# Optimization experiments

Measured on AMD Instinct MI355X. Metric: run time of the kernel, lower is better.

Reference implementation:

```python
import jax, jax.numpy as jnp
import numpy as np

BLOCK = 32  # mxfp8 block size along K


def setup_inputs() -> dict:
    key = jax.random.key(0)
    ks = jax.random.split(key, 7)
    TOK, IN, OUT, RANK = 8192, 4096, 4096, 64
    return {
        "input": jax.random.normal(ks[0], (TOK, IN), dtype=jnp.float32),
        "weight_q": jax.random.normal(ks[1], (OUT, IN), dtype=jnp.float32),
        "block_scale": jax.random.uniform(ks[2], (OUT, IN // BLOCK), dtype=jnp.float32),
        "bias": jax.random.normal(ks[3], (OUT,), dtype=jnp.float32),
        "svd_u": jax.random.normal(ks[4], (OUT, RANK), dtype=jnp.float32),
        "svd_s": jax.random.uniform(ks[5], (RANK,), dtype=jnp.float32),
        "svd_v": jax.random.normal(ks[6], (IN, RANK), dtype=jnp.float32),
    }


def _dequant_mxfp8(weight_q, block_scale):
    # weight_q: [M, K], block_scale: [M, K//BLOCK] -> per-block scaled weight [M, K]
    M, K = weight_q.shape
    nb = K // BLOCK
    w = weight_q.reshape(M, nb, BLOCK) * block_scale.reshape(M, nb, 1)
    return w.reshape(M, K)


def reference(input, weight_q, block_scale, bias, svd_u, svd_s, svd_v):
    # SVD outlier branch: ((input @ V) * S) @ U^T
    outlier = ((input @ svd_v) * svd_s[None, :]) @ svd_u.T  # [TOK, OUT]
    # Dequantize mxfp8 weight then linear: input @ W^T + bias
    w = _dequant_mxfp8(weight_q, block_scale)
    residual = input @ w.T + bias[None, :]
    return outlier + residual
```

## Files before the change

### kernel.cpp

```cpp
#include <hip/hip_runtime.h>
#include <stdint.h>

typedef unsigned short ushort_t;
typedef __attribute__((ext_vector_type(8))) short short8;
typedef __attribute__((ext_vector_type(4))) unsigned short ushort4_t;
typedef __attribute__((ext_vector_type(8))) unsigned short ushort8;
typedef __attribute__((ext_vector_type(4))) float f32x4;

#define TOK 8192
#define DIM_IN 4096
#define DIM_OUT 4096
#define RANK 64
#define NT (DIM_IN / 64)

__device__ __forceinline__ ushort_t f2bf(float f) {
    unsigned u = __float_as_uint(f);
    unsigned r = (u + 0x7fffu + ((u >> 16) & 1u)) >> 16;
    return (ushort_t)r;
}
__device__ __forceinline__ float bf2f(ushort_t u) {
    return __uint_as_float(((unsigned)u) << 16);
}

__device__ __forceinline__ void gload16(const void* g, void* l) {
    __builtin_amdgcn_global_load_lds(
        (const __attribute__((address_space(1))) unsigned int*)g,
        (__attribute__((address_space(3))) unsigned int*)l,
        16, 0, 0);
}

__global__ __launch_bounds__(256) void prep_input_k(const float* __restrict__ in,
                                                    ushort_t* __restrict__ out) {
    size_t idx = (size_t)blockIdx.x * 256 + threadIdx.x;
    const float4* p = (const float4*)(in + idx * 8);
    float4 f0 = p[0], f1 = p[1];
    ushort8 o;
    o[0] = f2bf(f0.x); o[1] = f2bf(f0.y); o[2] = f2bf(f0.z); o[3] = f2bf(f0.w);
    o[4] = f2bf(f1.x); o[5] = f2bf(f1.y); o[6] = f2bf(f1.z); o[7] = f2bf(f1.w);
    *(ushort8*)(out + idx * 8) = o;
}

__global__ __launch_bounds__(256) void prep_weight_k(const float* __restrict__ wq,
                                                     const float* __restrict__ scale,
                                                     const float* __restrict__ U,
                                                     const float* __restrict__ s,
                                                     const float* __restrict__ V,
                                                     ushort_t* __restrict__ Wb) {
    __shared__ ushort_t sm[18432];
    const int tid = threadIdx.x;
    const int wv = tid >> 6;
    const int lane = tid & 63;
    const int ob = blockIdx.x >> 5;
    const int kb = blockIdx.x & 31;

    char* smb = (char*)sm;
#pragma unroll
    for (int j = 0; j < 8; ++j) {
        int idx = j * 256 + tid;
        int row = idx >> 4;
        int c4 = idx & 15;
        float4 sv = *(const float4*)&s[c4 * 4];
        float4 u = *(const float4*)&U[(size_t)(ob * 128 + row) * RANK + c4 * 4];
        ushort4_t up;
        up[0] = f2bf(u.x * sv.x); up[1] = f2bf(u.y * sv.y);
        up[2] = f2bf(u.z * sv.z); up[3] = f2bf(u.w * sv.w);
        int wbyte = row * 128 + ((c4 * 8) ^ ((row & 7) << 4));
        *(ushort4_t*)(smb + wbyte) = up;
        float4 v = *(const float4*)&V[(size_t)(kb * 128 + row) * RANK + c4 * 4];
        ushort4_t vp;
        vp[0] = f2bf(v.x); vp[1] = f2bf(v.y); vp[2] = f2bf(v.z); vp[3] = f2bf(v.w);
        *(ushort4_t*)(smb + 16384 + wbyte) = vp;
    }
    __syncthreads();

    const int wr = wv >> 1, wc = wv & 1;
    f32x4 acc[4][4] = {};
    {
        short8 a[4], b[4];
#pragma unroll
        for (int kk = 0; kk < 2; ++kk) {
#pragma unroll
            for (int f = 0; f < 4; ++f) {
                int r = wr * 64 + f * 16 + (lane & 15);
                int kbyte = ((lane >> 4) * 16 + kk * 64) ^ ((r & 7) << 4);
                a[f] = *(const short8*)(smb + r * 128 + kbyte);
                int r2 = wc * 64 + f * 16 + (lane & 15);
                int kbyte2 = ((lane >> 4) * 16 + kk * 64) ^ ((r2 & 7) << 4);
                b[f] = *(const short8*)(smb + 16384 + r2 * 128 + kbyte2);
            }
#pragma unroll
            for (int fm = 0; fm < 4; ++fm)
#pragma unroll
                for (int fn = 0; fn < 4; ++fn)
                    acc[fm][fn] = __builtin_amdgcn_mfma_f32_16x16x32_bf16(
                        a[fm], b[fn], acc[fm][fn], 0, 0, 0);
        }
    }
    __syncthreads();

#pragma unroll
    for (int fm = 0; fm < 4; ++fm)
#pragma unroll
        for (int fn = 0; fn < 4; ++fn) {
            int row0 = wr * 64 + fm * 16 + (lane >> 4) * 4;
            int col = wc * 64 + fn * 16 + (lane & 15);
#pragma unroll
            for (int r = 0; r < 4; ++r)
                sm[(row0 + r) * 136 + col] = f2bf(acc[fm][fn][r]);
        }
    __syncthreads();

    const int ty = tid >> 4, tx = tid & 15;
#pragma unroll
    for (int i = 0; i < 8; ++i) {
        int ol = ty * 8 + i;
        int o = ob * 128 + ol;
        int k0 = kb * 128 + tx * 8;
        float sc = scale[(size_t)o * (DIM_IN / 32) + (k0 >> 5)];
        float4 q0 = *(const float4*)&wq[(size_t)o * DIM_IN + k0];
        float4 q1 = *(const float4*)&wq[(size_t)o * DIM_IN + k0 + 4];
        ushort8 sv8 = *(const ushort8*)&sm[ol * 136 + tx * 8];
        ushort8 w;
        w[0] = f2bf(q0.x * sc + bf2f(sv8[0]));
        w[1] = f2bf(q0.y * sc + bf2f(sv8[1]));
        w[2] = f2bf(q0.z * sc + bf2f(sv8[2]));
        w[3] = f2bf(q0.w * sc + bf2f(sv8[3]));
        w[4] = f2bf(q1.x * sc + bf2f(sv8[4]));
        w[5] = f2bf(q1.y * sc + bf2f(sv8[5]));
        w[6] = f2bf(q1.z * sc + bf2f(sv8[6]));
        w[7] = f2bf(q1.w * sc + bf2f(sv8[7]));
        *(ushort8*)&Wb[(size_t)o * DIM_IN + k0] = w;
    }
}

__global__ __launch_bounds__(512, 2) void gemm_k(const ushort_t* __restrict__ A,
                                                 const ushort_t* __restrict__ B,
                                                 const float* __restrict__ bias,
                                                 float* __restrict__ C) {
    __shared__ ushort_t lds[2][2][2][8192];

    const int tid = threadIdx.x;
    const int wid = tid >> 6;
    const int lane = tid & 63;

    int bid = blockIdx.x;
    int swz = (bid & 7) * 64 + (bid >> 3);
    const int bm = swz >> 4;
    const int bn = swz & 15;

    const int wr = wid >> 2;
    const int wc = wid & 3;

    const int lane2 = lane ^ (((lane >> 5) & 1) << 1);
    const int srow = (wid >> 1) * 16 + (lane2 >> 2);
    const int scol = (wid & 1) * 32 + (lane2 & 3) * 8;
    const ushort_t* pa = A + (size_t)(bm * 256 + srow) * DIM_IN + scol;
    const ushort_t* pb = B + (size_t)(bn * 256 + srow) * DIM_IN + scol;

    const int loff = ((((lane & 15) * 64 + (lane >> 4) * 16) ^ (((lane >> 3) & 1) << 5)) >> 1);

    f32x4 acc[8][4] = {};

    auto stageA = [&](int buf, int half, int t) {
        const ushort_t* g = pa + (size_t)half * 128 * DIM_IN + t * 64;
        gload16(g, &lds[buf][0][half][wid * 512]);
        gload16(g + (size_t)64 * DIM_IN, &lds[buf][0][half][(wid + 8) * 512]);
    };
    auto stageB = [&](int buf, int half, int t) {
        const ushort_t* g = pb + (size_t)half * 128 * DIM_IN + t * 64;
        gload16(g, &lds[buf][1][half][wid * 512]);
        gload16(g + (size_t)64 * DIM_IN, &lds[buf][1][half][(wid + 8) * 512]);
    };

    auto tile_step = [&](int buf, int t, int mode) {
        const ushort_t* LA = &lds[buf][0][wr][0];
        const ushort_t* LB = &lds[buf][1][wc >> 1][0];
        const int bsub = (wc & 1) * 4;
        short8 aA[4], aB[4], bA[2][2], bB[2][2];

        auto rdA = [&](short8 (&dst)[4], int mhalf, int kk) {
#pragma unroll
            for (int m = 0; m < 4; ++m)
                dst[m] = *(const short8*)(LA + ((((mhalf * 4 + m) * 2) + kk) << 9) + loff);
        };
        auto rdB = [&](short8 (&dst)[2][2], int noff, int kk) {
#pragma unroll
            for (int n = 0; n < 2; ++n)
                dst[n][kk] = *(const short8*)(LB + ((((bsub + noff + n) * 2) + kk) << 9) + loff);
        };
        auto cluster = [&](short8 (&av)[4], short8 (&bv)[2][2], int kk, int mb, int nb) {
            __builtin_amdgcn_s_setprio(1);
#pragma unroll
            for (int m = 0; m < 4; ++m)
#pragma unroll
                for (int n = 0; n < 2; ++n)
                    acc[mb + m][nb + n] =
                        __builtin_amdgcn_mfma_f32_16x16x32_bf16(av[m], bv[n][kk], acc[mb + m][nb + n], 0, 0, 0);
            __builtin_amdgcn_s_setprio(0);
        };

        rdA(aA, 0, 0);
        rdB(bA, 0, 0);
        rdA(aB, 0, 1);
        rdB(bA, 0, 1);
        if (mode >= 1) stageA(buf ^ 1, 1, t + 1);
        cluster(aA, bA, 0, 0, 0);
        rdB(bB, 2, 0);
        cluster(aB, bA, 1, 0, 0);

        rdB(bB, 2, 1);
        cluster(aA, bB, 0, 0, 2);
        rdA(aA, 1, 0);
        cluster(aB, bB, 1, 0, 2);
        __builtin_amdgcn_s_barrier();

        rdA(aB, 1, 1);
        if (mode == 2) { stageB(buf, 0, t + 2); stageB(buf, 1, t + 2); }
        cluster(aA, bB, 0, 4, 2);
        cluster(aB, bB, 1, 4, 2);
        __builtin_amdgcn_s_barrier();

        if (mode == 2) stageA(buf, 0, t + 2);
        cluster(aA, bA, 0, 4, 0);
        cluster(aB, bA, 1, 4, 0);
        if (mode == 2)
            asm volatile("s_waitcnt vmcnt(6)" ::: "memory");
        else if (mode == 1)
            asm volatile("s_waitcnt vmcnt(0)" ::: "memory");
        if (mode >= 1) __builtin_amdgcn_s_barrier();
    };

    stageA(0, 0, 0); stageA(0, 1, 0); stageB(0, 0, 0); stageB(0, 1, 0);
    stageB(1, 0, 1); stageB(1, 1, 1); stageA(1, 0, 1);
    asm volatile("s_waitcnt vmcnt(6)" ::: "memory");
    __builtin_amdgcn_s_barrier();

    for (int t = 0; t < NT - 2; t += 2) {
        tile_step(0, t, 2);
        tile_step(1, t + 1, 2);
    }
    tile_step(0, NT - 2, 1);
    tile_step(1, NT - 1, 0);

    const int ccol = lane & 15;
    const int crow = (lane >> 4) * 4;
#pragma unroll
    for (int n = 0; n < 4; ++n) {
        int gcol = bn * 256 + wc * 64 + n * 16 + ccol;
        float bv = bias[gcol];
#pragma unroll
        for (int m = 0; m < 8; ++m) {
            size_t grow = (size_t)(bm * 256 + wr * 128 + m * 16 + crow);
#pragma unroll
            for (int r = 0; r < 4; ++r)
                C[(grow + r) * DIM_OUT + gcol] = acc[m][n][r] + bv;
        }
    }
}

extern "C" void kernel_launch(void* const* d_in, const int* in_sizes, int n_in,
                              void* d_out, int out_size, void* d_ws, size_t ws_size,
                              hipStream_t stream) {
    const float* input = (const float*)d_in[0];
    const float* wq    = (const float*)d_in[1];
    const float* scale = (const float*)d_in[2];
    const float* bias  = (const float*)d_in[3];
    const float* U     = (const float*)d_in[4];
    const float* s     = (const float*)d_in[5];
    const float* V     = (const float*)d_in[6];
    float* out = (float*)d_out;

    ushort_t* Abf = (ushort_t*)d_ws;
    ushort_t* Wbf = Abf + (size_t)TOK * DIM_IN;

    prep_input_k<<<(TOK * DIM_IN) / (256 * 8), 256, 0, stream>>>(input, Abf);
    prep_weight_k<<<(DIM_OUT / 128) * (DIM_IN / 128), 256, 0, stream>>>(wq, scale, U, s, V, Wbf);
    gemm_k<<<(TOK / 256) * (DIM_OUT / 256), 512, 0, stream>>>(Abf, Wbf, bias, out);
}
```

Baseline: 286.7 us.

## Simplify GEMM to 256x128 tiles with 4 waves and K=32 double buffering

Replaces the 256x256 block tile (8 waves, hand-interleaved MFMA clusters and staggered async loads over K=64 stages) with a 256x128 tile using 4 waves and a plain double-buffered loop over K=32 stages. Each iteration loads all A/B fragments then issues 32 MFMAs, waiting for all outstanding loads and barriering per stage. This reduces scheduling complexity and LDS use, but halves the B-tile reuse per block, doubles the number of k-steps and barriers, and loses the fine-grained overlap of loads with compute.

```diff
diff --git a/kernel.cpp b/kernel.cpp
--- a/kernel.cpp
+++ b/kernel.cpp
@@ -11,7 +11,7 @@
 #define DIM_IN 4096
 #define DIM_OUT 4096
 #define RANK 64
-#define NT (DIM_IN / 64)
+#define NT32 (DIM_IN / 32)
 
 __device__ __forceinline__ ushort_t f2bf(float f) {
     unsigned u = __float_as_uint(f);
@@ -133,120 +133,83 @@
     }
 }
 
-__global__ __launch_bounds__(512, 2) void gemm_k(const ushort_t* __restrict__ A,
+__global__ __launch_bounds__(256, 2) void gemm_k(const ushort_t* __restrict__ A,
                                                  const ushort_t* __restrict__ B,
                                                  const float* __restrict__ bias,
                                                  float* __restrict__ C) {
-    __shared__ ushort_t lds[2][2][2][8192];
+    __shared__ ushort_t lds[2][12288];
 
     const int tid = threadIdx.x;
     const int wid = tid >> 6;
     const int lane = tid & 63;
 
     int bid = blockIdx.x;
-    int swz = (bid & 7) * 64 + (bid >> 3);
-    const int bm = swz >> 4;
-    const int bn = swz & 15;
-
-    const int wr = wid >> 2;
-    const int wc = wid & 3;
+    int swz = (bid & 7) * 128 + (bid >> 3);
+    const int bm = swz >> 5;
+    const int bn = swz & 31;
+
+    const int wr = wid >> 1;
+    const int wc = wid & 1;
 
     const int lane2 = lane ^ (((lane >> 5) & 1) << 1);
-    const int srow = (wid >> 1) * 16 + (lane2 >> 2);
-    const int scol = (wid & 1) * 32 + (lane2 & 3) * 8;
-    const ushort_t* pa = A + (size_t)(bm * 256 + srow) * DIM_IN + scol;
-    const ushort_t* pb = B + (size_t)(bn * 256 + srow) * DIM_IN + scol;
+    const int sr = lane2 >> 2;
+    const int sc = (lane2 & 3) * 8;
+    const ushort_t* pa = A + (size_t)(bm * 256 + sr) * DIM_IN + sc;
+    const ushort_t* pb = B + (size_t)(bn * 128 + sr) * DIM_IN + sc;
 
     const int loff = ((((lane & 15) * 64 + (lane >> 4) * 16) ^ (((lane >> 3) & 1) << 5)) >> 1);
 
     f32x4 acc[8][4] = {};
 
-    auto stageA = [&](int buf, int half, int t) {
-        const ushort_t* g = pa + (size_t)half * 128 * DIM_IN + t * 64;
-        gload16(g, &lds[buf][0][half][wid * 512]);
-        gload16(g + (size_t)64 * DIM_IN, &lds[buf][0][half][(wid + 8) * 512]);
+    auto stage = [&](int buf, int t) {
+#pragma unroll
+        for (int j = 0; j < 4; ++j) {
+            int s = wid * 4 + j;
+            gload16(pa + (size_t)(s * 16) * DIM_IN + t * 32, &lds[buf][s * 512]);
+        }
+#pragma unroll
+        for (int j = 0; j < 2; ++j) {
+            int s = wid * 2 + j;
+            gload16(pb + (size_t)(s * 16) * DIM_IN + t * 32, &lds[buf][8192 + s * 512]);
+        }
     };
-    auto stageB = [&](int buf, int half, int t) {
-        const ushort_t* g = pb + (size_t)half * 128 * DIM_IN + t * 64;
-        gload16(g, &lds[buf][1][half][wid * 512]);
-        gload16(g + (size_t)64 * DIM_IN, &lds[buf][1][half][(wid + 8) * 512]);
-    };
-
-    auto tile_step = [&](int buf, int t, int mode) {
-        const ushort_t* LA = &lds[buf][0][wr][0];
-        const ushort_t* LB = &lds[buf][1][wc >> 1][0];
-        const int bsub = (wc & 1) * 4;
-        short8 aA[4], aB[4], bA[2][2], bB[2][2];
-
-        auto rdA = [&](short8 (&dst)[4], int mhalf, int kk) {
-#pragma unroll
-            for (int m = 0; m < 4; ++m)
-                dst[m] = *(const short8*)(LA + ((((mhalf * 4 + m) * 2) + kk) << 9) + loff);
-        };
-        auto rdB = [&](short8 (&dst)[2][2], int noff, int kk) {
-#pragma unroll
-            for (int n = 0; n < 2; ++n)
-                dst[n][kk] = *(const short8*)(LB + ((((bsub + noff + n) * 2) + kk) << 9) + loff);
-        };
-        auto cluster = [&](short8 (&av)[4], short8 (&bv)[2][2], int kk, int mb, int nb) {
-            __builtin_amdgcn_s_setprio(1);
-#pragma unroll
-            for (int m = 0; m < 4; ++m)
-#pragma unroll
-                for (int n = 0; n < 2; ++n)
-                    acc[mb + m][nb + n] =
-                        __builtin_amdgcn_mfma_f32_16x16x32_bf16(av[m], bv[n][kk], acc[mb + m][nb + n], 0, 0, 0);
-            __builtin_amdgcn_s_setprio(0);
-        };
-
-        rdA(aA, 0, 0);
-        rdB(bA, 0, 0);
-        rdA(aB, 0, 1);
-        rdB(bA, 0, 1);
-        if (mode >= 1) stageA(buf ^ 1, 1, t + 1);
-        cluster(aA, bA, 0, 0, 0);
-        rdB(bB, 2, 0);
-        cluster(aB, bA, 1, 0, 0);
-
-        rdB(bB, 2, 1);
-        cluster(aA, bB, 0, 0, 2);
-        rdA(aA, 1, 0);
-        cluster(aB, bB, 1, 0, 2);
-        __builtin_amdgcn_s_barrier();
-
-        rdA(aB, 1, 1);
-        if (mode == 2) { stageB(buf, 0, t + 2); stageB(buf, 1, t + 2); }
-        cluster(aA, bB, 0, 4, 2);
-        cluster(aB, bB, 1, 4, 2);
-        __builtin_amdgcn_s_barrier();
-
-        if (mode == 2) stageA(buf, 0, t + 2);
-        cluster(aA, bA, 0, 4, 0);
-        cluster(aB, bA, 1, 4, 0);
-        if (mode == 2)
-            asm volatile("s_waitcnt vmcnt(6)" ::: "memory");
-        else if (mode == 1)
+
+    stage(0, 0);
+    asm volatile("s_waitcnt vmcnt(0)" ::: "memory");
+    __builtin_amdgcn_s_barrier();
+
+    for (int t = 0; t < NT32; ++t) {
+        const int cur = t & 1;
+        if (t + 1 < NT32) stage(cur ^ 1, t + 1);
+
+        const ushort_t* L = &lds[cur][0];
+        short8 a[8], b[4];
+#pragma unroll
+        for (int m = 0; m < 8; ++m)
+            a[m] = *(const short8*)(L + (wr * 8 + m) * 512 + loff);
+#pragma unroll
+        for (int n = 0; n < 4; ++n)
+            b[n] = *(const short8*)(L + 8192 + (wc * 4 + n) * 512 + loff);
+
+        __builtin_amdgcn_s_setprio(1);
+#pragma unroll
+        for (int m = 0; m < 8; ++m)
+#pragma unroll
+            for (int n = 0; n < 4; ++n)
+                acc[m][n] = __builtin_amdgcn_mfma_f32_16x16x32_bf16(a[m], b[n], acc[m][n], 0, 0, 0);
+        __builtin_amdgcn_s_setprio(0);
+
+        if (t + 1 < NT32) {
             asm volatile("s_waitcnt vmcnt(0)" ::: "memory");
-        if (mode >= 1) __builtin_amdgcn_s_barrier();
-    };
-
-    stageA(0, 0, 0); stageA(0, 1, 0); stageB(0, 0, 0); stageB(0, 1, 0);
-    stageB(1, 0, 1); stageB(1, 1, 1); stageA(1, 0, 1);
-    asm volatile("s_waitcnt vmcnt(6)" ::: "memory");
-    __builtin_amdgcn_s_barrier();
-
-    for (int t = 0; t < NT - 2; t += 2) {
-        tile_step(0, t, 2);
-        tile_step(1, t + 1, 2);
-    }
-    tile_step(0, NT - 2, 1);
-    tile_step(1, NT - 1, 0);
+            __builtin_amdgcn_s_barrier();
+        }
+    }
 
     const int ccol = lane & 15;
     const int crow = (lane >> 4) * 4;
 #pragma unroll
     for (int n = 0; n < 4; ++n) {
-        int gcol = bn * 256 + wc * 64 + n * 16 + ccol;
+        int gcol = bn * 128 + wc * 64 + n * 16 + ccol;
         float bv = bias[gcol];
 #pragma unroll
         for (int m = 0; m < 8; ++m) {
@@ -275,5 +238,5 @@
 
     prep_input_k<<<(TOK * DIM_IN) / (256 * 8), 256, 0, stream>>>(input, Abf);
     prep_weight_k<<<(DIM_OUT / 128) * (DIM_IN / 128), 256, 0, stream>>>(wq, scale, U, s, V, Wbf);
-    gemm_k<<<(TOK / 256) * (DIM_OUT / 256), 512, 0, stream>>>(Abf, Wbf, bias, out);
-}
+    gemm_k<<<(TOK / 256) * (DIM_OUT / 128), 256, 0, stream>>>(Abf, Wbf, bias, out);
+}
```

Result: slower. 362.8 us (+26.5%).

## Replace interleaved staged prefetch with simple double-buffered stage/consume loop

Applied to the files above, without the earlier changes.

Replaces the finely interleaved schedule, where A and B tile loads for later K-steps were issued between MFMA clusters with mid-tile barriers, with a plain double-buffer loop. Each iteration now consumes the current buffer, hits a barrier, then issues all eight loads for tile t+2 into that buffer before waiting. This simplifies synchronisation and removes the intra-tile barriers. In exchange, global loads are no longer spread across the MFMA work and the wait comes right after issuing the loads, so latency hiding may be weaker.

```diff
diff --git a/kernel.cpp b/kernel.cpp
--- a/kernel.cpp
+++ b/kernel.cpp
@@ -161,18 +161,19 @@
 
     f32x4 acc[8][4] = {};
 
-    auto stageA = [&](int buf, int half, int t) {
-        const ushort_t* g = pa + (size_t)half * 128 * DIM_IN + t * 64;
-        gload16(g, &lds[buf][0][half][wid * 512]);
-        gload16(g + (size_t)64 * DIM_IN, &lds[buf][0][half][(wid + 8) * 512]);
+    auto stage = [&](int buf, int t) {
+#pragma unroll
+        for (int half = 0; half < 2; ++half) {
+            const ushort_t* ga = pa + (size_t)half * 128 * DIM_IN + t * 64;
+            gload16(ga, &lds[buf][0][half][wid * 512]);
+            gload16(ga + (size_t)64 * DIM_IN, &lds[buf][0][half][(wid + 8) * 512]);
+            const ushort_t* gb = pb + (size_t)half * 128 * DIM_IN + t * 64;
+            gload16(gb, &lds[buf][1][half][wid * 512]);
+            gload16(gb + (size_t)64 * DIM_IN, &lds[buf][1][half][(wid + 8) * 512]);
+        }
     };
-    auto stageB = [&](int buf, int half, int t) {
-        const ushort_t* g = pb + (size_t)half * 128 * DIM_IN + t * 64;
-        gload16(g, &lds[buf][1][half][wid * 512]);
-        gload16(g + (size_t)64 * DIM_IN, &lds[buf][1][half][(wid + 8) * 512]);
-    };
-
-    auto tile_step = [&](int buf, int t, int mode) {
+
+    auto consume = [&](int buf) {
         const ushort_t* LA = &lds[buf][0][wr][0];
         const ushort_t* LB = &lds[buf][1][wc >> 1][0];
         const int bsub = (wc & 1) * 4;
@@ -203,44 +204,38 @@
         rdB(bA, 0, 0);
         rdA(aB, 0, 1);
         rdB(bA, 0, 1);
-        if (mode >= 1) stageA(buf ^ 1, 1, t + 1);
         cluster(aA, bA, 0, 0, 0);
         rdB(bB, 2, 0);
         cluster(aB, bA, 1, 0, 0);
-
         rdB(bB, 2, 1);
         cluster(aA, bB, 0, 0, 2);
         rdA(aA, 1, 0);
         cluster(aB, bB, 1, 0, 2);
-        __builtin_amdgcn_s_barrier();
-
         rdA(aB, 1, 1);
-        if (mode == 2) { stageB(buf, 0, t + 2); stageB(buf, 1, t + 2); }
         cluster(aA, bB, 0, 4, 2);
         cluster(aB, bB, 1, 4, 2);
-        __builtin_amdgcn_s_barrier();
-
-        if (mode == 2) stageA(buf, 0, t + 2);
         cluster(aA, bA, 0, 4, 0);
         cluster(aB, bA, 1, 4, 0);
-        if (mode == 2)
-            asm volatile("s_waitcnt vmcnt(6)" ::: "memory");
-        else if (mode == 1)
+    };
+
+    stage(0, 0);
+    stage(1, 1);
+    asm volatile("s_waitcnt vmcnt(8)" ::: "memory");
+    __builtin_amdgcn_s_barrier();
+
+    for (int t = 0; t < NT; ++t) {
+        const int cur = t & 1;
+        consume(cur);
+        if (t == NT - 1) break;
+        if (t + 2 < NT) {
+            __builtin_amdgcn_s_barrier();
+            stage(cur, t + 2);
+            asm volatile("s_waitcnt vmcnt(8)" ::: "memory");
+        } else {
             asm volatile("s_waitcnt vmcnt(0)" ::: "memory");
-        if (mode >= 1) __builtin_amdgcn_s_barrier();
-    };
-
-    stageA(0, 0, 0); stageA(0, 1, 0); stageB(0, 0, 0); stageB(0, 1, 0);
-    stageB(1, 0, 1); stageB(1, 1, 1); stageA(1, 0, 1);
-    asm volatile("s_waitcnt vmcnt(6)" ::: "memory");
-    __builtin_amdgcn_s_barrier();
-
-    for (int t = 0; t < NT - 2; t += 2) {
-        tile_step(0, t, 2);
-        tile_step(1, t + 1, 2);
-    }
-    tile_step(0, NT - 2, 1);
-    tile_step(1, NT - 1, 0);
+        }
+        __builtin_amdgcn_s_barrier();
+    }
 
     const int ccol = lane & 15;
     const int crow = (lane >> 4) * 4;
```

Result: slower. 335.3 us (+16.9%).
